# Kernel tuning notes

Hardware: AMD Instinct MI355X
Metric: run time of the kernel (lower is better)

The kernel has to match this reference:

```python
import jax, jax.numpy as jnp
import numpy as np
from jax import lax

SEQ, BATCH, VOCAB, EMB, HID = 256, 64, 32000, 1024, 1024


def _lstm_layer(xs, w_ih, w_hh, b_ih, b_hh):
    """Single-direction LSTM layer, time-major xs: [S, B, E] -> (ys [S,B,H], h [B,H], c [B,H]).
    PyTorch gate order: i, f, g, o."""
    S, B, _ = xs.shape
    H = w_hh.shape[1]
    # Precompute input projection for all timesteps (one big GEMM).
    x_proj = jnp.einsum('sbe,ge->sbg', xs, w_ih) + b_ih + b_hh  # [S, B, 4H]

    def step(carry, xp):
        h, c = carry
        gates = xp + h @ w_hh.T  # [B, 4H]
        i, f, g, o = jnp.split(gates, 4, axis=-1)
        i = jax.nn.sigmoid(i)
        f = jax.nn.sigmoid(f)
        g = jnp.tanh(g)
        o = jax.nn.sigmoid(o)
        c = f * c + i * g
        h = o * jnp.tanh(c)
        return (h, c), h

    h0 = jnp.zeros((B, H), dtype=xs.dtype)
    c0 = jnp.zeros((B, H), dtype=xs.dtype)
    (h, c), ys = lax.scan(step, (h0, c0), x_proj)
    return ys, h, c


def setup_inputs() -> dict:
    key = jax.random.key(0)
    ks = jax.random.split(key, 10)
    d = {
        'input_seq': jax.random.randint(ks[0], (SEQ, BATCH), 0, VOCAB, dtype=jnp.int64 if jax.config.jax_enable_x64 else jnp.int32),
        'emb': jax.random.normal(ks[1], (VOCAB, EMB), dtype=jnp.float32),
        'w_ih_0': jax.random.normal(ks[2], (4 * HID, EMB), dtype=jnp.float32) * 0.05,
        'w_hh_0': jax.random.normal(ks[3], (4 * HID, HID), dtype=jnp.float32) * 0.05,
        'b_ih_0': jax.random.normal(ks[4], (4 * HID,), dtype=jnp.float32) * 0.05,
        'b_hh_0': jax.random.normal(ks[5], (4 * HID,), dtype=jnp.float32) * 0.05,
        'w_ih_1': jax.random.normal(ks[6], (4 * HID, HID), dtype=jnp.float32) * 0.05,
        'w_hh_1': jax.random.normal(ks[7], (4 * HID, HID), dtype=jnp.float32) * 0.05,
        'b_ih_1': jax.random.normal(ks[8], (4 * HID,), dtype=jnp.float32) * 0.05,
        'b_hh_1': jax.random.normal(ks[9], (4 * HID,), dtype=jnp.float32) * 0.05,
    }
    return d


def reference(input_seq, emb, w_ih_0, w_hh_0, b_ih_0, b_hh_0, w_ih_1, w_hh_1, b_ih_1, b_hh_1):
    x = emb[input_seq]  # [S, B, E] embedding gather
    ys0, h0, c0 = _lstm_layer(x, w_ih_0, w_hh_0, b_ih_0, b_hh_0)
    ys1, h1, c1 = _lstm_layer(ys0, w_ih_1, w_hh_1, b_ih_1, b_hh_1)
    h_n = jnp.stack([h0, h1])  # [num_layers, B, H]
    c_n = jnp.stack([c0, c1])
    return (h_n, c_n)
```

## Files before the change

### kernel.cpp

```cpp
#include <hip/hip_runtime.h>
#include <hip/hip_bf16.h>

typedef __attribute__((ext_vector_type(8))) short bf16x8;
typedef __attribute__((ext_vector_type(4))) float f32x4;

__device__ __forceinline__ ushort f2b(float f) {
    union { float f; unsigned u; } v; v.f = f;
    unsigned r = v.u + 0x7FFFu + ((v.u >> 16) & 1u);
    return (ushort)(r >> 16);
}
__device__ __forceinline__ float b2f(ushort u) {
    union { unsigned u; float f; } v; v.u = ((unsigned)u) << 16;
    return v.f;
}
__device__ __forceinline__ float sigm(float x) {
    return 1.f / (1.f + __expf(-x));
}

#define HLOAD(dst, p, off) \
    asm volatile("global_load_dwordx4 %0, %1, off offset:" #off " sc0 sc1" \
                 : "=v"(dst) : "v"(p))
#define HSTORE(p, v) \
    asm volatile("global_store_dword %0, %1, off sc0 sc1" \
                 :: "v"(p), "v"(v) : "memory")

__global__ __launch_bounds__(256) void prep_weights(
    const float* __restrict__ wih0, const float* __restrict__ whh0,
    const float* __restrict__ bih0, const float* __restrict__ bhh0,
    const float* __restrict__ wih1, const float* __restrict__ whh1,
    const float* __restrict__ bih1, const float* __restrict__ bhh1,
    ushort* __restrict__ wih0b, ushort* __restrict__ whh0b,
    ushort* __restrict__ wih1b, ushort* __restrict__ whh1b,
    float* __restrict__ bsum0, float* __restrict__ bsum1)
{
    const int i = blockIdx.x * 256 + threadIdx.x;
    const int e = i * 4;
    float4 v;
    v = *(const float4*)&wih0[e];
    *(ushort4*)&wih0b[e] = make_ushort4(f2b(v.x), f2b(v.y), f2b(v.z), f2b(v.w));
    v = *(const float4*)&whh0[e];
    *(ushort4*)&whh0b[e] = make_ushort4(f2b(v.x), f2b(v.y), f2b(v.z), f2b(v.w));
    v = *(const float4*)&wih1[e];
    *(ushort4*)&wih1b[e] = make_ushort4(f2b(v.x), f2b(v.y), f2b(v.z), f2b(v.w));
    v = *(const float4*)&whh1[e];
    *(ushort4*)&whh1b[e] = make_ushort4(f2b(v.x), f2b(v.y), f2b(v.z), f2b(v.w));
    if (i < 1024) {
        const int b4 = i * 4;
        float4 a0 = *(const float4*)&bih0[b4];
        float4 b0 = *(const float4*)&bhh0[b4];
        *(float4*)&bsum0[b4] = make_float4(a0.x + b0.x, a0.y + b0.y, a0.z + b0.z, a0.w + b0.w);
        float4 a1 = *(const float4*)&bih1[b4];
        float4 b1 = *(const float4*)&bhh1[b4];
        *(float4*)&bsum1[b4] = make_float4(a1.x + b1.x, a1.y + b1.y, a1.z + b1.z, a1.w + b1.w);
    }
}

__global__ __launch_bounds__(256) void gather_x(
    const int* __restrict__ idx, const float* __restrict__ emb,
    ushort* __restrict__ xg)
{
    const int row = blockIdx.x;
    const int c = threadIdx.x;
    const int v = idx[row];
    const float4 f = *(const float4*)&emb[(size_t)v * 1024u + c * 4];
    *(ushort4*)&xg[(size_t)row * 1024u + c * 4] =
        make_ushort4(f2b(f.x), f2b(f.y), f2b(f.z), f2b(f.w));
}

__global__ __launch_bounds__(256) void inproj_mfma(
    const ushort* __restrict__ A, const ushort* __restrict__ W,
    const float* __restrict__ bsum, ushort* __restrict__ xpout, int mbase)
{
    __shared__ ushort As[128][72];
    __shared__ ushort Bsh[128][72];
    const int tid = threadIdx.x;
    const int wv = tid >> 6, lane = tid & 63;
    const int l15 = lane & 15, l4 = lane >> 4;
    const int m0 = blockIdx.y * 128, n0 = blockIdx.x * 128;
    const int wm = (wv & 1) * 64, wn = (wv >> 1) * 64;

    f32x4 acc[4][4];
    #pragma unroll
    for (int i = 0; i < 4; ++i)
        #pragma unroll
        for (int j = 0; j < 4; ++j) acc[i][j] = (f32x4){0.f, 0.f, 0.f, 0.f};

    for (int k0 = 0; k0 < 1024; k0 += 64) {
        __syncthreads();
        #pragma unroll
        for (int s4 = 0; s4 < 4; ++s4) {
            const int s = tid + s4 * 256;
            const int row = s >> 3, c8 = (s & 7) * 8;
            *(bf16x8*)&As[row][c8] =
                *(const bf16x8*)&A[(size_t)(mbase + m0 + row) * 1024u + k0 + c8];
            *(bf16x8*)&Bsh[row][c8] =
                *(const bf16x8*)&W[(size_t)(n0 + row) * 1024u + k0 + c8];
        }
        __syncthreads();
        #pragma unroll
        for (int kk = 0; kk < 2; ++kk) {
            bf16x8 af[4], bfr[4];
            #pragma unroll
            for (int i = 0; i < 4; ++i) {
                af[i]  = *(const bf16x8*)&As[wm + i * 16 + l15][kk * 32 + l4 * 8];
                bfr[i] = *(const bf16x8*)&Bsh[wn + i * 16 + l15][kk * 32 + l4 * 8];
            }
            #pragma unroll
            for (int i = 0; i < 4; ++i)
                #pragma unroll
                for (int j = 0; j < 4; ++j)
                    acc[i][j] = __builtin_amdgcn_mfma_f32_16x16x32_bf16(
                        af[i], bfr[j], acc[i][j], 0, 0, 0);
        }
    }
    #pragma unroll
    for (int i = 0; i < 4; ++i) {
        const int m = m0 + wm + i * 16 + l4 * 4;
        #pragma unroll
        for (int j = 0; j < 4; ++j) {
            const int g = n0 + wn + j * 16 + l15;
            const float bs = bsum[g];
            #pragma unroll
            for (int r = 0; r < 4; ++r)
                xpout[(size_t)(m + r) * 4096u + g] = f2b(acc[i][j][r] + bs);
        }
    }
}

__global__ __launch_bounds__(256) void lstm_persist(
    const ushort* __restrict__ Whh,
    const ushort* __restrict__ xp,
    ushort* __restrict__ hbuf,
    float* __restrict__ cbuf,
    ushort* __restrict__ ys,
    float* __restrict__ outHC,
    unsigned* __restrict__ flags,
    int t0, int nt, int layer)
{
    __shared__ ushort Ws[32][1032];
    __shared__ float red[4][4][2][64][4];
    __shared__ float gs[4][16][33];

    const int tid = threadIdx.x;
    const int wv = tid >> 6, lane = tid & 63;
    const int l15 = lane & 15, l4 = lane >> 4;
    const int bid = blockIdx.x;
    const int hc0 = bid * 8;

    for (int s = tid; s < 32 * 128; s += 256) {
        const int row = s >> 7, c8 = (s & 127) * 8;
        const int g = (row & 3) * 1024 + hc0 + (row >> 2);
        *(bf16x8*)&Ws[row][c8] = *(const bf16x8*)&Whh[(size_t)g * 1024u + c8];
    }

    const int pb = wv * 16 + (lane >> 2);
    const int pp = lane & 3;
    float cs[2];
    if (t0 == 0) { cs[0] = cs[1] = 0.f; }
    else {
        float2 c2 = *(const float2*)&cbuf[(size_t)pb * 1024u + hc0 + 2 * pp];
        cs[0] = c2.x; cs[1] = c2.y;
    }
    __syncthreads();

    const int kbase = wv * 256;
    const unsigned* xpu = (const unsigned*)xp;
    const int pl = wv * 32 + (lane & 31);

    for (int ts = 0; ts < nt; ++ts) {
        const int t = t0 + ts;
        const unsigned need = (unsigned)(layer * 256 + t);
        const ushort* hr = hbuf + (size_t)(t & 1) * 65536u;

        unsigned xq[4];
        #pragma unroll
        for (int q = 0; q < 4; ++q)
            xq[q] = xpu[(size_t)(ts * 64 + pb) * 2048u + q * 512 + (hc0 >> 1) + pp];

        for (;;) {
            const unsigned f = __hip_atomic_load(&flags[pl], __ATOMIC_RELAXED, __HIP_MEMORY_SCOPE_AGENT);
            if (__all(f >= need)) break;
            __builtin_amdgcn_s_sleep(1);
        }

        bf16x8 hf[8][4];
        const ushort* rb[4];
        #pragma unroll
        for (int i = 0; i < 4; ++i)
            rb[i] = hr + (size_t)(i * 16 + l15) * 1024u + kbase + l4 * 8;
        #pragma unroll
        for (int i = 0; i < 4; ++i) {
            HLOAD(hf[0][i], rb[i], 0);
            HLOAD(hf[1][i], rb[i], 64);
            HLOAD(hf[2][i], rb[i], 128);
            HLOAD(hf[3][i], rb[i], 192);
            HLOAD(hf[4][i], rb[i], 256);
            HLOAD(hf[5][i], rb[i], 320);
            HLOAD(hf[6][i], rb[i], 384);
            HLOAD(hf[7][i], rb[i], 448);
        }
        asm volatile("s_waitcnt vmcnt(0)" ::: "memory");
        __builtin_amdgcn_sched_barrier(0);

        f32x4 acc[4][2];
        #pragma unroll
        for (int i = 0; i < 4; ++i) {
            acc[i][0] = (f32x4){0.f, 0.f, 0.f, 0.f};
            acc[i][1] = (f32x4){0.f, 0.f, 0.f, 0.f};
        }
        #pragma unroll
        for (int kk = 0; kk < 8; ++kk) {
            const int k = kbase + kk * 32 + l4 * 8;
            bf16x8 bf0 = *(const bf16x8*)&Ws[l15][k];
            bf16x8 bf1 = *(const bf16x8*)&Ws[16 + l15][k];
            #pragma unroll
            for (int i = 0; i < 4; ++i) {
                acc[i][0] = __builtin_amdgcn_mfma_f32_16x16x32_bf16(hf[kk][i], bf0, acc[i][0], 0, 0, 0);
                acc[i][1] = __builtin_amdgcn_mfma_f32_16x16x32_bf16(hf[kk][i], bf1, acc[i][1], 0, 0, 0);
            }
        }

        #pragma unroll
        for (int i = 0; i < 4; ++i) {
            if (i != wv) {
                *(f32x4*)&red[i][wv][0][lane][0] = acc[i][0];
                *(f32x4*)&red[i][wv][1][lane][0] = acc[i][1];
            }
        }
        __syncthreads();
        f32x4 fin0 = (f32x4){0.f,0.f,0.f,0.f}, fin1 = (f32x4){0.f,0.f,0.f,0.f};
        #pragma unroll
        for (int i = 0; i < 4; ++i)
            if (i == wv) { fin0 = acc[i][0]; fin1 = acc[i][1]; }
        #pragma unroll
        for (int src = 0; src < 4; ++src) {
            if (src != wv) {
                fin0 += *(const f32x4*)&red[wv][src][0][lane][0];
                fin1 += *(const f32x4*)&red[wv][src][1][lane][0];
            }
        }

        #pragma unroll
        for (int r = 0; r < 4; ++r) {
            gs[wv][l4 * 4 + r][l15]      = fin0[r];
            gs[wv][l4 * 4 + r][16 + l15] = fin1[r];
        }

        ushort* hw = hbuf + (size_t)((t + 1) & 1) * 65536u;
        float hv[2];
        #pragma unroll
        for (int d = 0; d < 2; ++d) {
            const int grow = (2 * pp + d) * 4;
            const float g0 = gs[wv][lane >> 2][grow + 0] + b2f((ushort)(d ? (xq[0] >> 16) : (xq[0] & 0xffff)));
            const float g1 = gs[wv][lane >> 2][grow + 1] + b2f((ushort)(d ? (xq[1] >> 16) : (xq[1] & 0xffff)));
            const float g2 = gs[wv][lane >> 2][grow + 2] + b2f((ushort)(d ? (xq[2] >> 16) : (xq[2] & 0xffff)));
            const float g3 = gs[wv][lane >> 2][grow + 3] + b2f((ushort)(d ? (xq[3] >> 16) : (xq[3] & 0xffff)));
            const float ig = sigm(g0), fg = sigm(g1);
            const float gg = tanhf(g2), og = sigm(g3);
            const float c = fg * cs[d] + ig * gg;
            hv[d] = og * tanhf(c);
            cs[d] = c;
        }
        const unsigned hpack = (unsigned)f2b(hv[0]) | ((unsigned)f2b(hv[1]) << 16);
        unsigned* hwp = (unsigned*)(hw + (size_t)pb * 1024u + hc0 + 2 * pp);
        HSTORE(hwp, hpack);
        asm volatile("s_waitcnt vmcnt(0)" ::: "memory");
        __syncthreads();
        if (tid == 0)
            __hip_atomic_store(&flags[bid], need + 1, __ATOMIC_RELAXED, __HIP_MEMORY_SCOPE_AGENT);

        if (ys)
            *(unsigned*)(ys + (size_t)(t * 64 + pb) * 1024u + hc0 + 2 * pp) = hpack;
        if (t == 255) {
            #pragma unroll
            for (int d = 0; d < 2; ++d) {
                const int hc = hc0 + 2 * pp + d;
                outHC[(size_t)layer * 65536u + (size_t)pb * 1024u + hc] = hv[d];
                outHC[131072u + (size_t)layer * 65536u + (size_t)pb * 1024u + hc] = cs[d];
            }
        }
    }

    *(float2*)&cbuf[(size_t)pb * 1024u + hc0 + 2 * pp] = make_float2(cs[0], cs[1]);
}

extern "C" void kernel_launch(void* const* d_in, const int* in_sizes, int n_in,
                              void* d_out, int out_size, void* d_ws, size_t ws_size,
                              hipStream_t stream) {
    (void)in_sizes; (void)n_in; (void)out_size; (void)ws_size;
    const int*   idx  = (const int*)d_in[0];
    const float* emb  = (const float*)d_in[1];
    const float* wih[2] = {(const float*)d_in[2], (const float*)d_in[6]};
    const float* whh[2] = {(const float*)d_in[3], (const float*)d_in[7]};
    const float* bih[2] = {(const float*)d_in[4], (const float*)d_in[8]};
    const float* bhh[2] = {(const float*)d_in[5], (const float*)d_in[9]};
    float* out = (float*)d_out;

    char* p = (char*)d_ws;
    ushort* xg    = (ushort*)p;  p += 33554432;
    ushort* ys0   = (ushort*)p;  p += 33554432;
    ushort* wihb0 = (ushort*)p;  p += 8388608;
    ushort* whhb0 = (ushort*)p;  p += 8388608;
    ushort* wihb1 = (ushort*)p;  p += 8388608;
    ushort* whhb1 = (ushort*)p;  p += 8388608;
    ushort* xp    = (ushort*)p;  p += 33554432;
    ushort* hbuf  = (ushort*)p;  p += 262144;
    float*  cbuf  = (float*)p;   p += 262144;
    float*  bsum0 = (float*)p;   p += 16384;
    float*  bsum1 = (float*)p;   p += 16384;
    unsigned* flags = (unsigned*)p;

    hipMemsetAsync(flags, 0, 512, stream);
    prep_weights<<<4096, 256, 0, stream>>>(
        wih[0], whh[0], bih[0], bhh[0], wih[1], whh[1], bih[1], bhh[1],
        wihb0, whhb0, wihb1, whhb1, bsum0, bsum1);
    gather_x<<<16384, 256, 0, stream>>>(idx, emb, xg);

    const ushort* wihbL[2] = {wihb0, wihb1};
    const ushort* whhbL[2] = {whhb0, whhb1};
    const float*  bsumL[2] = {bsum0, bsum1};

    for (int L = 0; L < 2; ++L) {
        hipMemsetAsync(hbuf, 0, 262144, stream);
        const ushort* Abase = (L == 0) ? xg : ys0;
        ushort* ysout = (L == 0) ? ys0 : nullptr;
        for (int ch = 0; ch < 4; ++ch) {
            inproj_mfma<<<dim3(32, 32), 256, 0, stream>>>(
                Abase, wihbL[L], bsumL[L], xp, ch * 4096);
            lstm_persist<<<128, 256, 0, stream>>>(
                whhbL[L], xp, hbuf, cbuf, ysout, out, flags, ch * 64, 64, L);
        }
    }
}
```

Measured before the change: 4.505 ms.

## Split persistent LSTM work by batch per wave with per-wave flags

Each wave now computes the full K=1024 reduction for its own 16 batch rows, instead of every wave taking a K-slice over all 64 rows. This removes the LDS cross-wave reduction and one block barrier per timestep. Completion is signalled per wave with its own flag (512 flags), and consumers poll them with vectorized loads. The h loads are issued in staged groups of 8, with partial vmcnt waits so MFMAs overlap the remaining loads. The cost is more h data loaded per wave and more flags to poll on each spin.

```diff
diff --git a/kernel.cpp b/kernel.cpp
--- a/kernel.cpp
+++ b/kernel.cpp
@@ -3,6 +3,7 @@
 
 typedef __attribute__((ext_vector_type(8))) short bf16x8;
 typedef __attribute__((ext_vector_type(4))) float f32x4;
+typedef __attribute__((ext_vector_type(4))) unsigned u32x4;
 
 __device__ __forceinline__ ushort f2b(float f) {
     union { float f; unsigned u; } v; v.f = f;
@@ -127,7 +128,7 @@
     }
 }
 
-__global__ __launch_bounds__(256) void lstm_persist(
+__global__ __launch_bounds__(256, 1) void lstm_persist(
     const ushort* __restrict__ Whh,
     const ushort* __restrict__ xp,
     ushort* __restrict__ hbuf,
@@ -138,7 +139,6 @@
     int t0, int nt, int layer)
 {
     __shared__ ushort Ws[32][1032];
-    __shared__ float red[4][4][2][64][4];
     __shared__ float gs[4][16][33];
 
     const int tid = threadIdx.x;
@@ -163,9 +163,9 @@
     }
     __syncthreads();
 
-    const int kbase = wv * 256;
     const unsigned* xpu = (const unsigned*)xp;
-    const int pl = wv * 32 + (lane & 31);
+    const u32x4* f4 = (const u32x4*)flags;
+    const int myflag = bid * 4 + wv;
 
     for (int ts = 0; ts < nt; ++ts) {
         const int t = t0 + ts;
@@ -178,72 +178,68 @@
             xq[q] = xpu[(size_t)(ts * 64 + pb) * 2048u + q * 512 + (hc0 >> 1) + pp];
 
         for (;;) {
-            const unsigned f = __hip_atomic_load(&flags[pl], __ATOMIC_RELAXED, __HIP_MEMORY_SCOPE_AGENT);
-            if (__all(f >= need)) break;
+            u32x4 fa, fb;
+            HLOAD(fa, f4 + lane, 0);
+            HLOAD(fb, f4 + lane, 1024);
+            asm volatile("s_waitcnt vmcnt(0)" ::: "memory");
+            __builtin_amdgcn_sched_barrier(0);
+            unsigned mna = min(min(fa[0], fa[1]), min(fa[2], fa[3]));
+            unsigned mnb = min(min(fb[0], fb[1]), min(fb[2], fb[3]));
+            if (__all(min(mna, mnb) >= need)) break;
             __builtin_amdgcn_s_sleep(1);
         }
 
-        bf16x8 hf[8][4];
-        const ushort* rb[4];
-        #pragma unroll
-        for (int i = 0; i < 4; ++i)
-            rb[i] = hr + (size_t)(i * 16 + l15) * 1024u + kbase + l4 * 8;
-        #pragma unroll
-        for (int i = 0; i < 4; ++i) {
-            HLOAD(hf[0][i], rb[i], 0);
-            HLOAD(hf[1][i], rb[i], 64);
-            HLOAD(hf[2][i], rb[i], 128);
-            HLOAD(hf[3][i], rb[i], 192);
-            HLOAD(hf[4][i], rb[i], 256);
-            HLOAD(hf[5][i], rb[i], 320);
-            HLOAD(hf[6][i], rb[i], 384);
-            HLOAD(hf[7][i], rb[i], 448);
-        }
+        bf16x8 hf[32];
+        const ushort* rbase = hr + (size_t)(wv * 16 + l15) * 1024u + l4 * 8;
+        HLOAD(hf[0],  rbase, 0);    HLOAD(hf[1],  rbase, 64);
+        HLOAD(hf[2],  rbase, 128);  HLOAD(hf[3],  rbase, 192);
+        HLOAD(hf[4],  rbase, 256);  HLOAD(hf[5],  rbase, 320);
+        HLOAD(hf[6],  rbase, 384);  HLOAD(hf[7],  rbase, 448);
+        HLOAD(hf[8],  rbase, 512);  HLOAD(hf[9],  rbase, 576);
+        HLOAD(hf[10], rbase, 640);  HLOAD(hf[11], rbase, 704);
+        HLOAD(hf[12], rbase, 768);  HLOAD(hf[13], rbase, 832);
+        HLOAD(hf[14], rbase, 896);  HLOAD(hf[15], rbase, 960);
+        HLOAD(hf[16], rbase, 1024); HLOAD(hf[17], rbase, 1088);
+        HLOAD(hf[18], rbase, 1152); HLOAD(hf[19], rbase, 1216);
+        HLOAD(hf[20], rbase, 1280); HLOAD(hf[21], rbase, 1344);
+        HLOAD(hf[22], rbase, 1408); HLOAD(hf[23], rbase, 1472);
+        HLOAD(hf[24], rbase, 1536); HLOAD(hf[25], rbase, 1600);
+        HLOAD(hf[26], rbase, 1664); HLOAD(hf[27], rbase, 1728);
+        HLOAD(hf[28], rbase, 1792); HLOAD(hf[29], rbase, 1856);
+        HLOAD(hf[30], rbase, 1920); HLOAD(hf[31], rbase, 1984);
+
+        f32x4 acc0 = (f32x4){0.f, 0.f, 0.f, 0.f};
+        f32x4 acc1 = (f32x4){0.f, 0.f, 0.f, 0.f};
+
+#define MFMA_GRP(G) \
+        _Pragma("unroll") \
+        for (int kk2 = 0; kk2 < 8; ++kk2) { \
+            const int kk = (G) * 8 + kk2; \
+            const int k = kk * 32 + l4 * 8; \
+            bf16x8 b0 = *(const bf16x8*)&Ws[l15][k]; \
+            bf16x8 b1 = *(const bf16x8*)&Ws[16 + l15][k]; \
+            acc0 = __builtin_amdgcn_mfma_f32_16x16x32_bf16(hf[kk], b0, acc0, 0, 0, 0); \
+            acc1 = __builtin_amdgcn_mfma_f32_16x16x32_bf16(hf[kk], b1, acc1, 0, 0, 0); \
+        }
+
+        asm volatile("s_waitcnt vmcnt(24)" ::: "memory");
+        __builtin_amdgcn_sched_barrier(0);
+        MFMA_GRP(0)
+        asm volatile("s_waitcnt vmcnt(16)" ::: "memory");
+        __builtin_amdgcn_sched_barrier(0);
+        MFMA_GRP(1)
+        asm volatile("s_waitcnt vmcnt(8)" ::: "memory");
+        __builtin_amdgcn_sched_barrier(0);
+        MFMA_GRP(2)
         asm volatile("s_waitcnt vmcnt(0)" ::: "memory");
         __builtin_amdgcn_sched_barrier(0);
-
-        f32x4 acc[4][2];
-        #pragma unroll
-        for (int i = 0; i < 4; ++i) {
-            acc[i][0] = (f32x4){0.f, 0.f, 0.f, 0.f};
-            acc[i][1] = (f32x4){0.f, 0.f, 0.f, 0.f};
-        }
-        #pragma unroll
-        for (int kk = 0; kk < 8; ++kk) {
-            const int k = kbase + kk * 32 + l4 * 8;
-            bf16x8 bf0 = *(const bf16x8*)&Ws[l15][k];
-            bf16x8 bf1 = *(const bf16x8*)&Ws[16 + l15][k];
-            #pragma unroll
-            for (int i = 0; i < 4; ++i) {
-                acc[i][0] = __builtin_amdgcn_mfma_f32_16x16x32_bf16(hf[kk][i], bf0, acc[i][0], 0, 0, 0);
-                acc[i][1] = __builtin_amdgcn_mfma_f32_16x16x32_bf16(hf[kk][i], bf1, acc[i][1], 0, 0, 0);
-            }
-        }
-
-        #pragma unroll
-        for (int i = 0; i < 4; ++i) {
-            if (i != wv) {
-                *(f32x4*)&red[i][wv][0][lane][0] = acc[i][0];
-                *(f32x4*)&red[i][wv][1][lane][0] = acc[i][1];
-            }
-        }
-        __syncthreads();
-        f32x4 fin0 = (f32x4){0.f,0.f,0.f,0.f}, fin1 = (f32x4){0.f,0.f,0.f,0.f};
-        #pragma unroll
-        for (int i = 0; i < 4; ++i)
-            if (i == wv) { fin0 = acc[i][0]; fin1 = acc[i][1]; }
-        #pragma unroll
-        for (int src = 0; src < 4; ++src) {
-            if (src != wv) {
-                fin0 += *(const f32x4*)&red[wv][src][0][lane][0];
-                fin1 += *(const f32x4*)&red[wv][src][1][lane][0];
-            }
-        }
+        MFMA_GRP(3)
+#undef MFMA_GRP
 
         #pragma unroll
         for (int r = 0; r < 4; ++r) {
-            gs[wv][l4 * 4 + r][l15]      = fin0[r];
-            gs[wv][l4 * 4 + r][16 + l15] = fin1[r];
+            gs[wv][l4 * 4 + r][l15]      = acc0[r];
+            gs[wv][l4 * 4 + r][16 + l15] = acc1[r];
         }
 
         ushort* hw = hbuf + (size_t)((t + 1) & 1) * 65536u;
@@ -265,9 +261,11 @@
         unsigned* hwp = (unsigned*)(hw + (size_t)pb * 1024u + hc0 + 2 * pp);
         HSTORE(hwp, hpack);
         asm volatile("s_waitcnt vmcnt(0)" ::: "memory");
-        __syncthreads();
-        if (tid == 0)
-            __hip_atomic_store(&flags[bid], need + 1, __ATOMIC_RELAXED, __HIP_MEMORY_SCOPE_AGENT);
+
+        if (lane == 0) {
+            unsigned* fp = &flags[myflag];
+            HSTORE(fp, need + 1);
+        }
 
         if (ys)
             *(unsigned*)(ys + (size_t)(t * 64 + pb) * 1024u + hc0 + 2 * pp) = hpack;
@@ -310,7 +308,7 @@
     float*  bsum1 = (float*)p;   p += 16384;
     unsigned* flags = (unsigned*)p;
 
-    hipMemsetAsync(flags, 0, 512, stream);
+    hipMemsetAsync(flags, 0, 2048, stream);
     prep_weights<<<4096, 256, 0, stream>>>(
         wih[0], whh[0], bih[0], bhh[0], wih[1], whh[1], bih[1], bhh[1],
         wihb0, whhb0, wihb1, whhb1, bsum0, bsum1);
```

New measurement: 5.444 ms. 1.21x slower.
